# Kernel tuning notes

Measured on AMD Instinct MI355X. Metric: run time of the kernel, lower is better.

## Reference

```python
import jax, jax.numpy as jnp
import numpy as np

PAD_IDX = 0
B, T, S, H, V = 64, 32, 64, 1024, 32000


def setup_inputs() -> dict:
    key = jax.random.key(0)
    ks = jax.random.split(key, 12)
    s = 0.02
    emb_tbl = jax.random.normal(ks[0], (V, H), jnp.float32) * s
    emb_tbl = emb_tbl.at[PAD_IDX].set(0.0)  # padding_idx row is zero
    return {
        "input": jax.random.randint(ks[1], (B, T), 0, V),
        "memory": jax.random.normal(ks[2], (1, B, H), jnp.float32),
        "encoder_output": jax.random.normal(ks[3], (B, S, H), jnp.float32),
        "xs_len": jax.random.randint(ks[4], (B,), 1, S + 1),
        "embedding": emb_tbl,
        "w_ih": jax.random.normal(ks[5], (3 * H, 2 * H), jnp.float32) * s,
        "w_hh": jax.random.normal(ks[6], (3 * H, H), jnp.float32) * s,
        "b_ih": jnp.zeros((3 * H,), jnp.float32),
        "b_hh": jnp.zeros((3 * H,), jnp.float32),
        "l1": jax.random.normal(ks[7], (H, H), jnp.float32) * s,
        "l2": jax.random.normal(ks[8], (H, 2 * H), jnp.float32) * s,
        "w_out": jax.random.normal(ks[9], (V, H), jnp.float32) * s,
        "b_out": jnp.zeros((V,), jnp.float32),
    }


def _gru_cell(x, h, w_ih, w_hh, b_ih, b_hh):
    # torch.nn.GRUCell math
    gi = x @ w_ih.T + b_ih          # [B, 3H]
    gh = h @ w_hh.T + b_hh          # [B, 3H]
    ir, iz, inn = jnp.split(gi, 3, axis=1)
    hr, hz, hn = jnp.split(gh, 3, axis=1)
    r = jax.nn.sigmoid(ir + hr)
    z = jax.nn.sigmoid(iz + hz)
    n = jnp.tanh(inn + r * hn)
    return (1.0 - z) * n + z * h


def _attention(hidden, enc, seq_mask, l1, l2):
    # hidden: [B,H], enc: [B,S,H], seq_mask: [B,S] float {0,1}
    q = hidden @ l1.T                              # [B,H]
    score = jnp.einsum("bsh,bh->bs", enc, q)       # [B,S]
    masked = seq_mask * score
    # faithful to `masked_att[masked_att == 0] = -1e10`
    masked = jnp.where(masked == 0.0, -1e10, masked)
    attn = jax.nn.softmax(masked, axis=1)          # softmax over source positions
    ctx = jnp.einsum("bs,bsh->bh", attn, enc)      # [B,H]
    out = jnp.tanh(jnp.concatenate([ctx, hidden], axis=1) @ l2.T)
    return out, attn


def reference(input, memory, encoder_output, xs_len, embedding,
              w_ih, w_hh, b_ih, b_hh, l1, l2, w_out, b_out):
    emb = embedding[input]                         # [B,T,H]
    emb_t = jnp.swapaxes(emb, 0, 1)                # [T,B,H]
    h0 = memory[0]                                 # [B,H]
    ctx0 = jnp.zeros_like(h0)
    s_len = encoder_output.shape[1]
    seq_mask = (jnp.arange(s_len)[None, :] < xs_len[:, None]).astype(emb.dtype)  # [B,S]

    def step(carry, e_t):
        h_prev, ctx = carry
        x = jnp.concatenate([e_t, ctx], axis=1)    # [B,2H]
        h = _gru_cell(x, h_prev, w_ih, w_hh, b_ih, b_hh)
        ctx_new, attn = _attention(h, encoder_output, seq_mask, l1, l2)
        scores = jax.nn.log_softmax(ctx_new @ w_out.T + b_out, axis=1)  # [B,V]
        return (h, ctx_new), (scores, attn)

    (h_fin, ctx_fin), (all_scores, all_attn) = jax.lax.scan(step, (h0, ctx0), emb_t)
    decoder_output = jnp.swapaxes(all_scores, 0, 1)        # [B,T,V]
    decoder_hidden = h_fin[None, :, :]                     # [1,B,H]
    attention_weights = jnp.swapaxes(all_attn, 0, 1)       # [B,T,S]
    return decoder_output, decoder_hidden, attention_weights, ctx_fin
```

## Files before the change

kernel.cpp:

```cpp
#include <hip/hip_runtime.h>


#define B_ 64
#define T_ 32
#define S_ 64
#define H_ 1024
#define V_ 32000
#define NB_ 256
#define LDS_BYTES 152064

#define HID_OFF 65536000L
#define ATT_OFF 65601536L
#define CTF_OFF 65732608L

typedef __attribute__((ext_vector_type(8))) short bf16x8;
typedef __attribute__((ext_vector_type(4))) float f32x4;
typedef __attribute__((ext_vector_type(4))) unsigned int u32x4;
typedef unsigned short u16;
typedef unsigned long long u64;

__device__ __forceinline__ u16 f2bf(float v) {
  unsigned int u = __float_as_uint(v);
  unsigned int r = (u + 0x7fffu + ((u >> 16) & 1u)) >> 16;
  return (u16)r;
}
__device__ __forceinline__ float bf2f(u16 h) {
  return __uint_as_float(((unsigned int)h) << 16);
}
__device__ __forceinline__ void split2(float v, u16* hi, u16* lo) {
  u16 h = f2bf(v);
  *hi = h;
  *lo = f2bf(v - bf2f(h));
}

__device__ __forceinline__ u64 aload_u64(const void* p) {
  return __hip_atomic_load((const u64*)p, __ATOMIC_RELAXED, __HIP_MEMORY_SCOPE_AGENT);
}
__device__ __forceinline__ unsigned aload_u32(const void* p) {
  return __hip_atomic_load((const unsigned*)p, __ATOMIC_RELAXED, __HIP_MEMORY_SCOPE_AGENT);
}
__device__ __forceinline__ void astore_u64(void* p, u64 v) {
  __hip_atomic_store((u64*)p, v, __ATOMIC_RELAXED, __HIP_MEMORY_SCOPE_AGENT);
}
__device__ __forceinline__ void astore_f32(float* p, float v) {
  __hip_atomic_store((unsigned*)p, __float_as_uint(v), __ATOMIC_RELAXED,
                     __HIP_MEMORY_SCOPE_AGENT);
}


__global__ void k_split(const float* __restrict__ src, u16* __restrict__ hi,
                        u16* __restrict__ lo, int n) {
  int i = blockIdx.x * blockDim.x + threadIdx.x;
  int stride = gridDim.x * blockDim.x;
  for (; i < n; i += stride) split2(src[i], &hi[i], &lo[i]);
}

__global__ void k_tobf(const float* __restrict__ src, u16* __restrict__ dst, int n) {
  int i = blockIdx.x * blockDim.x + threadIdx.x;
  int stride = gridDim.x * blockDim.x;
  for (; i < n; i += stride) dst[i] = f2bf(src[i]);
}

__global__ void k_l1t(const float* __restrict__ l1, u16* __restrict__ hi,
                      u16* __restrict__ lo) {
  __shared__ float tile[64][65];
  int it = blockIdx.x & 15, kt = blockIdx.x >> 4;
  for (int q = 0; q < 16; ++q) {
    int idx = q * 256 + threadIdx.x;
    int r = idx >> 6, c = idx & 63;
    tile[r][c] = l1[(long)(it * 64 + r) * H_ + kt * 64 + c];
  }
  __syncthreads();
  for (int q = 0; q < 16; ++q) {
    int idx = q * 256 + threadIdx.x;
    int r = idx >> 6, c = idx & 63;
    long o = (long)(kt * 64 + r) * H_ + it * 64 + c;
    split2(tile[c][r], &hi[o], &lo[o]);
  }
}

__global__ void k_embx(const int* __restrict__ inp, const float* __restrict__ emb,
                       u16* __restrict__ hi, u16* __restrict__ lo) {
  int bt = blockIdx.x;
  int b = bt >> 5, t = bt & 31;
  int id = inp[b * T_ + t];
  const float* src = emb + (long)id * H_;
  long base = (long)(t * B_ + b) * H_;
  for (int k = threadIdx.x; k < H_; k += 256) split2(src[k], &hi[base + k], &lo[base + k]);
}

__global__ void k_h0(const float* __restrict__ mem, u16* __restrict__ hh,
                     u16* __restrict__ hl) {
  int i = blockIdx.x * 256 + threadIdx.x;
  float v = mem[i];
  split2(v, &hh[i], &hl[i]);
}

__global__ void k_guard(float* out, float v) {
  if (blockIdx.x == 0 && threadIdx.x == 0) out[0] = v;
}

template <int SPLIT, int OMODE>
__launch_bounds__(256)
__global__ void k_gemm128(const u16* __restrict__ Ah, const u16* __restrict__ Al,
                          const u16* __restrict__ Bh, const u16* __restrict__ Bl,
                          float* __restrict__ C, const float* __restrict__ bias,
                          int Mtiles, int Ntiles, int K, int Arow, int Brow, int Crow) {
  (void)Ntiles;
  int bx = blockIdx.x;
  int mt = bx % Mtiles, nt = bx / Mtiles;
  int m0 = mt * 128, n0 = nt * 128;

  __shared__ __attribute__((aligned(16))) u16 lds[(SPLIT ? 4 : 2) * 4096];
  char* L = (char*)lds;
  const int tid = threadIdx.x;
  const int lane = tid & 63, wid = tid >> 6;
  const int wm = wid & 1, wn = wid >> 1;
  const int l15 = lane & 15, kq = lane >> 4;

  f32x4 acc[4][4];
  const f32x4 z4 = {0.f, 0.f, 0.f, 0.f};
#pragma unroll
  for (int i = 0; i < 4; ++i)
#pragma unroll
    for (int j = 0; j < 4; ++j) acc[i][j] = z4;

  const int ksteps = K >> 5;
  for (int kt = 0; kt < ksteps; ++kt) {
    __syncthreads();
#pragma unroll
    for (int h2 = 0; h2 < 2; ++h2) {
      int r = (tid >> 2) + (h2 << 6);
      int slot = tid & 3;
      int so = ((slot ^ (r & 3)) << 4);
      long ga = (long)(m0 + r) * Arow + (kt << 5) + (slot << 3);
      long gb = (long)(n0 + r) * Brow + (kt << 5) + (slot << 3);
      *(u32x4*)(L + r * 64 + so) = *(const u32x4*)(Ah + ga);
      *(u32x4*)(L + 8192 + r * 64 + so) = *(const u32x4*)(Bh + gb);
      if (SPLIT) {
        *(u32x4*)(L + 16384 + r * 64 + so) = *(const u32x4*)(Al + ga);
        *(u32x4*)(L + 24576 + r * 64 + so) = *(const u32x4*)(Bl + gb);
      }
    }
    __syncthreads();
    bf16x8 aH[4], bH[4], aL[4], bL[4];
#pragma unroll
    for (int mi = 0; mi < 4; ++mi) {
      int r = (wm << 6) + (mi << 4) + l15;
      int off = r * 64 + ((kq ^ (r & 3)) << 4);
      aH[mi] = *(const bf16x8*)(L + off);
      if (SPLIT) aL[mi] = *(const bf16x8*)(L + 16384 + off);
    }
#pragma unroll
    for (int ni = 0; ni < 4; ++ni) {
      int c = (wn << 6) + (ni << 4) + l15;
      int off = c * 64 + ((kq ^ (c & 3)) << 4);
      bH[ni] = *(const bf16x8*)(L + 8192 + off);
      if (SPLIT) bL[ni] = *(const bf16x8*)(L + 24576 + off);
    }
#pragma unroll
    for (int mi = 0; mi < 4; ++mi)
#pragma unroll
      for (int ni = 0; ni < 4; ++ni) {
        acc[mi][ni] = __builtin_amdgcn_mfma_f32_16x16x32_bf16(aH[mi], bH[ni], acc[mi][ni], 0, 0, 0);
        if (SPLIT) {
          acc[mi][ni] = __builtin_amdgcn_mfma_f32_16x16x32_bf16(aL[mi], bH[ni], acc[mi][ni], 0, 0, 0);
          acc[mi][ni] = __builtin_amdgcn_mfma_f32_16x16x32_bf16(aH[mi], bL[ni], acc[mi][ni], 0, 0, 0);
        }
      }
  }
#pragma unroll
  for (int mi = 0; mi < 4; ++mi)
#pragma unroll
    for (int ni = 0; ni < 4; ++ni)
#pragma unroll
      for (int e = 0; e < 4; ++e) {
        int r = (wm << 6) + (mi << 4) + (kq << 2) + e;
        int c = (wn << 6) + (ni << 4) + l15;
        int gm = m0 + r, gn = n0 + c;
        float v = acc[mi][ni][e];
        if (OMODE == 0) {
          C[(long)gm * Crow + gn] = v;
        } else {
          v += bias[gn];
          C[((long)(gm & 63) * T_ + (gm >> 6)) * V_ + gn] = v;
        }
      }
}

__device__ __forceinline__ void gridbar(unsigned* flags, unsigned seq) {
  __syncthreads();
  if (threadIdx.x == 0) {
    unsigned g = blockIdx.x & 7u;
    unsigned old = __hip_atomic_fetch_add(flags + g * 64, 1u, __ATOMIC_RELEASE,
                                          __HIP_MEMORY_SCOPE_AGENT);
    if (old == seq * 32u - 1u) {
      unsigned o2 = __hip_atomic_fetch_add(flags + 1024, 1u, __ATOMIC_RELEASE,
                                           __HIP_MEMORY_SCOPE_AGENT);
      if (o2 == seq * 8u - 1u)
        __hip_atomic_store(flags + 1040, seq, __ATOMIC_RELAXED,
                           __HIP_MEMORY_SCOPE_AGENT);
    }
    while (__hip_atomic_load(flags + 1040, __ATOMIC_RELAXED,
                             __HIP_MEMORY_SCOPE_AGENT) < seq)
      __builtin_amdgcn_s_sleep(2);
  }
  __syncthreads();
}

__launch_bounds__(256)
__global__ void k_rec(const float* __restrict__ embi,
                      u16* __restrict__ dctx_h, u16* __restrict__ dctx_l,
                      u16* __restrict__ hh_r, u16* __restrict__ hl_r,
                      const float* __restrict__ memory,
                      const u16* __restrict__ wih_h, const u16* __restrict__ wih_l,
                      const u16* __restrict__ whh_h, const u16* __restrict__ whh_l,
                      const u16* __restrict__ l2_h, const u16* __restrict__ l2_l,
                      float* __restrict__ gip, float* __restrict__ ghp,
                      float* __restrict__ psc, float* __restrict__ ctxp,
                      const float* __restrict__ encT, const float* __restrict__ encL,
                      const int* __restrict__ xs_len,
                      const float* __restrict__ bih, const float* __restrict__ bhh,
                      float* __restrict__ dout, unsigned* flags) {
  extern __shared__ __attribute__((aligned(16))) char L[];
  char* W_HI = L;
  char* W_LO = L + 65536;
  char* A_HI = L + 131072;
  char* A_LO = L + 139264;
  float* hq = (float*)(L + 147456);
  float* at_s = (float*)(L + 148480);
  const int bx = blockIdx.x;
  const int tid = threadIdx.x;
  const int lane = tid & 63, wid = tid >> 6;
  const int wm = wid & 1, wn = wid >> 1;
  const int l15 = lane & 15, kq = lane >> 4;
  const f32x4 z4 = {0.f, 0.f, 0.f, 0.f};
  unsigned seq = 1;

  const int isGI = (bx < 96);
  const int isGH = (bx >= 96 && bx < 192);
  const int isL2 = (bx >= 192 && bx < 224);
  const int sb = bx >> 2;
  const int sq = bx & 3;
  int nt = 0, kc = 0, n0 = 0;
  const u16 *Wg_h = nullptr, *Wg_l = nullptr;
  int wrs = 0;
  if (isGI) {
    nt = bx % 48; kc = bx / 48;
    Wg_h = wih_h + 1024 + (long)nt * 64 * 2048 + kc * 512;
    Wg_l = wih_l + 1024 + (long)nt * 64 * 2048 + kc * 512;
    wrs = 2048;
  } else if (isGH) {
    int j2 = bx - 96;
    nt = j2 % 48; kc = j2 / 48;
    Wg_h = whh_h + (long)nt * 64 * 1024 + kc * 512;
    Wg_l = whh_l + (long)nt * 64 * 1024 + kc * 512;
    wrs = 1024;
  } else if (isL2) {
    n0 = (bx - 192) << 5;
    Wg_h = l2_h + 1024 + (long)n0 * 2048;
    Wg_l = l2_l + 1024 + (long)n0 * 2048;
    wrs = 2048;
  }

  if (isGI || isGH) {
    for (int e = tid; e < 4096; e += 256) {
      int st = e >> 8, r = (e >> 2) & 63, slot = e & 3;
      long g = (long)r * wrs + st * 32 + slot * 8;
      int o = st * 4096 + r * 64 + ((slot ^ (r & 3)) << 4);
      *(u32x4*)(W_HI + o) = *(const u32x4*)(Wg_h + g);
      *(u32x4*)(W_LO + o) = *(const u32x4*)(Wg_l + g);
    }
  } else if (isL2) {
    for (int e = tid; e < 4096; e += 256) {
      int st = e >> 7, r = (e >> 2) & 31, slot = e & 3;
      long g = (long)r * wrs + st * 32 + slot * 8;
      int o = st * 2048 + r * 64 + ((slot ^ (r & 3)) << 4);
      *(u32x4*)(W_HI + o) = *(const u32x4*)(Wg_h + g);
      *(u32x4*)(W_LO + o) = *(const u32x4*)(Wg_l + g);
    }
  }
  __syncthreads();

  float hpv = memory[sb * 1024 + sq * 256 + tid];

  const int pr = tid >> 2, ps = tid & 3;
  const int ao = pr * 64 + ((ps ^ (pr & 3)) << 4);

  for (int t = 0; t < T_; ++t) {
    if (isGI || isGH) {
      const u16* Ah;
      const u16* Al;
      float* outp;
      if (isGI) {
        Ah = dctx_h + (long)t * 65536 + kc * 512;
        Al = dctx_l + (long)t * 65536 + kc * 512;
        outp = gip + (long)kc * 196608 + nt * 64;
      } else {
        Ah = hh_r + (long)t * 65536 + kc * 512;
        Al = hl_r + (long)t * 65536 + kc * 512;
        outp = ghp + (long)kc * 196608 + nt * 64;
      }
      const long g0 = (long)pr * 1024 + ps * 8;
      u32x4 ph0 = *(const u32x4*)(Ah + g0);
      u32x4 ph1 = *(const u32x4*)(Ah + g0 + 32);
      u32x4 pl0 = *(const u32x4*)(Al + g0);
      u32x4 pl1 = *(const u32x4*)(Al + g0 + 32);

      f32x4 acc[2][2];
#pragma unroll
      for (int i = 0; i < 2; ++i)
#pragma unroll
        for (int j = 0; j < 2; ++j) acc[i][j] = z4;

      for (int kt = 0; kt < 8; ++kt) {
        __syncthreads();
        *(u32x4*)(A_HI + ao) = ph0;
        *(u32x4*)(A_HI + 4096 + ao) = ph1;
        *(u32x4*)(A_LO + ao) = pl0;
        *(u32x4*)(A_LO + 4096 + ao) = pl1;
        __syncthreads();
        if (kt < 7) {
          long g = g0 + (kt + 1) * 64;
          ph0 = *(const u32x4*)(Ah + g);
          ph1 = *(const u32x4*)(Ah + g + 32);
          pl0 = *(const u32x4*)(Al + g);
          pl1 = *(const u32x4*)(Al + g + 32);
        }
#pragma unroll
        for (int sub = 0; sub < 2; ++sub) {
          const int stw = (kt * 2 + sub) * 4096;
          const int sta = sub * 4096;
          bf16x8 aH[2], aL[2], bH[2], bL[2];
#pragma unroll
          for (int mi = 0; mi < 2; ++mi) {
            int rr = (wm << 5) + (mi << 4) + l15;
            int off = rr * 64 + ((kq ^ (rr & 3)) << 4);
            aH[mi] = *(const bf16x8*)(A_HI + sta + off);
            aL[mi] = *(const bf16x8*)(A_LO + sta + off);
          }
#pragma unroll
          for (int ni = 0; ni < 2; ++ni) {
            int c = (wn << 5) + (ni << 4) + l15;
            int off = c * 64 + ((kq ^ (c & 3)) << 4);
            bH[ni] = *(const bf16x8*)(W_HI + stw + off);
            bL[ni] = *(const bf16x8*)(W_LO + stw + off);
          }
#pragma unroll
          for (int mi = 0; mi < 2; ++mi)
#pragma unroll
            for (int ni = 0; ni < 2; ++ni) {
              acc[mi][ni] = __builtin_amdgcn_mfma_f32_16x16x32_bf16(aH[mi], bH[ni], acc[mi][ni], 0, 0, 0);
              acc[mi][ni] = __builtin_amdgcn_mfma_f32_16x16x32_bf16(aL[mi], bH[ni], acc[mi][ni], 0, 0, 0);
              acc[mi][ni] = __builtin_amdgcn_mfma_f32_16x16x32_bf16(aH[mi], bL[ni], acc[mi][ni], 0, 0, 0);
            }
        }
      }
#pragma unroll
      for (int mi = 0; mi < 2; ++mi)
#pragma unroll
        for (int ni = 0; ni < 2; ++ni)
#pragma unroll
          for (int e = 0; e < 4; ++e) {
            int r = (wm << 5) + (mi << 4) + (kq << 2) + e;
            int c = (wn << 5) + (ni << 4) + l15;
            astore_f32(outp + (long)r * 3072 + c, acc[mi][ni][e]);
          }
    }
    gridbar(flags, seq); seq++;

    {
      const int b = sb, q = sq;
      const int j = (q << 8) + tid;
      const float* eb = embi + ((long)t * 64 + b) * 3072;
      float g0r = __uint_as_float(aload_u32(gip + b * 3072 + j));
      float g1r = __uint_as_float(aload_u32(gip + 196608 + b * 3072 + j));
      float g0z = __uint_as_float(aload_u32(gip + b * 3072 + 1024 + j));
      float g1z = __uint_as_float(aload_u32(gip + 196608 + b * 3072 + 1024 + j));
      float g0n = __uint_as_float(aload_u32(gip + b * 3072 + 2048 + j));
      float g1n = __uint_as_float(aload_u32(gip + 196608 + b * 3072 + 2048 + j));
      float h0r = __uint_as_float(aload_u32(ghp + b * 3072 + j));
      float h1r = __uint_as_float(aload_u32(ghp + 196608 + b * 3072 + j));
      float h0z = __uint_as_float(aload_u32(ghp + b * 3072 + 1024 + j));
      float h1z = __uint_as_float(aload_u32(ghp + 196608 + b * 3072 + 1024 + j));
      float h0n = __uint_as_float(aload_u32(ghp + b * 3072 + 2048 + j));
      float h1n = __uint_as_float(aload_u32(ghp + 196608 + b * 3072 + 2048 + j));
      float ir = eb[j] + g0r + g1r + bih[j];
      float iz = eb[1024 + j] + g0z + g1z + bih[1024 + j];
      float in2 = eb[2048 + j] + g0n + g1n + bih[2048 + j];
      float hr = h0r + h1r + bhh[j];
      float hz = h0z + h1z + bhh[1024 + j];
      float hn = h0n + h1n + bhh[2048 + j];
      float r = 1.f / (1.f + expf(-(ir + hr)));
      float z = 1.f / (1.f + expf(-(iz + hz)));
      float n = tanhf(in2 + r * hn);
      float h = (1.f - z) * n + z * hpv;
      hpv = h;
      hq[tid] = h;
      if (t == T_ - 1) dout[HID_OFF + (long)b * 1024 + j] = h;
      __syncthreads();
      if (tid < 64) {
        u64 ph = 0, pl = 0;
#pragma unroll
        for (int ii = 0; ii < 4; ++ii) {
          u16 hi, lo;
          split2(hq[tid * 4 + ii], &hi, &lo);
          ph |= (u64)hi << (16 * ii);
          pl |= (u64)lo << (16 * ii);
        }
        long o = (long)(t + 1) * 65536 + (long)b * 1024 + (q << 8) + tid * 4;
        astore_u64(hh_r + o, ph);
        astore_u64(hl_r + o, pl);
      }
      {
        int s = tid >> 2, part = tid & 3;
        const float4* ep = (const float4*)(encT + (((long)b * 64 + s) << 10) + (q << 8) + (part << 6));
        const float4* hp = (const float4*)(hq + (part << 6));
        float dot = 0.f;
#pragma unroll
        for (int kk = 0; kk < 16; ++kk) {
          float4 e = ep[kk], a = hp[kk];
          dot += e.x * a.x + e.y * a.y + e.z * a.z + e.w * a.w;
        }
        dot += __shfl_xor(dot, 1);
        dot += __shfl_xor(dot, 2);
        if (part == 0) astore_f32(psc + (((b << 2) + q) << 6) + s, dot);
      }
    }
    gridbar(flags, seq); seq++;

    {
      const int b = sb, q = sq;
      if (tid < 64) {
        int s = tid;
        float v = 0.f;
#pragma unroll
        for (int qq = 0; qq < 4; ++qq)
          v += __uint_as_float(aload_u32(psc + (((b << 2) + qq) << 6) + s));
        int len = xs_len[b];
        if (s >= len || v == 0.0f) v = -1e10f;
        float m = v;
#pragma unroll
        for (int off = 32; off; off >>= 1) m = fmaxf(m, __shfl_xor(m, off));
        float p = expf(v - m);
        float sum = p;
#pragma unroll
        for (int off = 32; off; off >>= 1) sum += __shfl_xor(sum, off);
        float a = p / sum;
        at_s[s] = a;
        if (q == 0) dout[ATT_OFF + ((long)b * T_ + t) * S_ + s] = a;
      }
      __syncthreads();
      {
        const float* lp = encL + (((long)b * 64 + (q << 4)) << 10) + tid * 4;
        float c0 = 0.f, c1 = 0.f, c2 = 0.f, c3 = 0.f;
#pragma unroll
        for (int s2 = 0; s2 < 16; ++s2) {
          float a = at_s[(q << 4) + s2];
          float4 e = *(const float4*)(lp + (s2 << 10));
          c0 += a * e.x; c1 += a * e.y; c2 += a * e.z; c3 += a * e.w;
        }
        u64 w0 = ((u64)__float_as_uint(c1) << 32) | __float_as_uint(c0);
        u64 w1 = ((u64)__float_as_uint(c3) << 32) | __float_as_uint(c2);
        long o = (((long)(b << 2) + q) << 10) + tid * 4;
        astore_u64(ctxp + o, w0);
        astore_u64(ctxp + o + 2, w1);
      }
    }
    gridbar(flags, seq); seq++;

    if (isL2) {
      const u16* Ah = hh_r + (long)(t + 1) * 65536;
      const u16* Al = hl_r + (long)(t + 1) * 65536;
      const long g0 = (long)pr * 1024 + ps * 8;
      u32x4 ph0 = *(const u32x4*)(Ah + g0);
      u32x4 ph1 = *(const u32x4*)(Ah + g0 + 32);
      u32x4 pl0 = *(const u32x4*)(Al + g0);
      u32x4 pl1 = *(const u32x4*)(Al + g0 + 32);

      f32x4 acc[2];
      acc[0] = z4; acc[1] = z4;
      for (int kt = 0; kt < 16; ++kt) {
        __syncthreads();
        *(u32x4*)(A_HI + ao) = ph0;
        *(u32x4*)(A_HI + 4096 + ao) = ph1;
        *(u32x4*)(A_LO + ao) = pl0;
        *(u32x4*)(A_LO + 4096 + ao) = pl1;
        __syncthreads();
        if (kt < 15) {
          long g = g0 + (kt + 1) * 64;
          ph0 = *(const u32x4*)(Ah + g);
          ph1 = *(const u32x4*)(Ah + g + 32);
          pl0 = *(const u32x4*)(Al + g);
          pl1 = *(const u32x4*)(Al + g + 32);
        }
#pragma unroll
        for (int sub = 0; sub < 2; ++sub) {
          const int stw = (kt * 2 + sub) * 2048;
          const int sta = sub * 4096;
          bf16x8 aH[2], aL[2], bH, bL;
#pragma unroll
          for (int mi = 0; mi < 2; ++mi) {
            int rr = (wm << 5) + (mi << 4) + l15;
            int off = rr * 64 + ((kq ^ (rr & 3)) << 4);
            aH[mi] = *(const bf16x8*)(A_HI + sta + off);
            aL[mi] = *(const bf16x8*)(A_LO + sta + off);
          }
          {
            int c = (wn << 4) + l15;
            int off = c * 64 + ((kq ^ (c & 3)) << 4);
            bH = *(const bf16x8*)(W_HI + stw + off);
            bL = *(const bf16x8*)(W_LO + stw + off);
          }
#pragma unroll
          for (int mi = 0; mi < 2; ++mi) {
            acc[mi] = __builtin_amdgcn_mfma_f32_16x16x32_bf16(aH[mi], bH, acc[mi], 0, 0, 0);
            acc[mi] = __builtin_amdgcn_mfma_f32_16x16x32_bf16(aL[mi], bH, acc[mi], 0, 0, 0);
            acc[mi] = __builtin_amdgcn_mfma_f32_16x16x32_bf16(aH[mi], bL, acc[mi], 0, 0, 0);
          }
        }
      }
      __syncthreads();
      float* cf = (float*)(L + 131072);
#pragma unroll
      for (int mi = 0; mi < 2; ++mi)
#pragma unroll
        for (int e = 0; e < 4; ++e) {
          int rr = (wm << 5) + (mi << 4) + (kq << 2) + e;
          int cc = (wn << 4) + l15;
          float a = 0.f;
#pragma unroll
          for (int qq = 0; qq < 4; ++qq)
            a += __uint_as_float(aload_u32(ctxp + (((long)(rr << 2) + qq) << 10) + n0 + cc));
          float v = tanhf(acc[mi][e] + a);
          if (t == T_ - 1) dout[CTF_OFF + (long)rr * 1024 + n0 + cc] = v;
          cf[rr * 32 + cc] = v;
        }
      __syncthreads();
#pragma unroll
      for (int qq2 = 0; qq2 < 2; ++qq2) {
        int g = tid + qq2 * 256;
        int b = g >> 3, colg = g & 7;
        u64 ph = 0, pl = 0;
#pragma unroll
        for (int ii = 0; ii < 4; ++ii) {
          float v = cf[b * 32 + colg * 4 + ii];
          u16 hi, lo;
          split2(v, &hi, &lo);
          ph |= (u64)hi << (16 * ii);
          pl |= (u64)lo << (16 * ii);
        }
        long o = (long)(t + 1) * 65536 + (long)b * 1024 + n0 + colg * 4;
        astore_u64(dctx_h + o, ph);
        astore_u64(dctx_l + o, pl);
      }
    }
    if (t < T_ - 1) { gridbar(flags, seq); }
    seq++;
  }
}

__device__ __forceinline__ void lse_comb(float& m, float& s, float mo, float so) {
  float M = fmaxf(m, mo);
  s = s * __expf(m - M) + so * __expf(mo - M);
  m = M;
}

__launch_bounds__(256)
__global__ void k_lsm(float* __restrict__ dout) {
  long base = (long)blockIdx.x * V_;
  int tid = threadIdx.x;
  float m = -3.0e38f, s = 0.f;
  for (int v = tid; v < V_; v += 256) {
    float x = dout[base + v];
    if (x > m) {
      s = s * __expf(m - x) + 1.f;
      m = x;
    } else {
      s += __expf(x - m);
    }
  }
#pragma unroll
  for (int off = 32; off; off >>= 1) {
    float mo = __shfl_xor(m, off), so = __shfl_xor(s, off);
    lse_comb(m, s, mo, so);
  }
  __shared__ float ms[4], ss[4];
  if ((tid & 63) == 0) { ms[tid >> 6] = m; ss[tid >> 6] = s; }
  __syncthreads();
  float M = ms[0], S = ss[0];
  for (int w2 = 1; w2 < 4; ++w2) lse_comb(M, S, ms[w2], ss[w2]);
  float logden = M + logf(S);
  for (int v = tid; v < V_; v += 256) dout[base + v] -= logden;
}

extern "C" void kernel_launch(void* const* d_in, const int* in_sizes, int n_in,
                              void* d_out, int out_size, void* d_ws, size_t ws_size,
                              hipStream_t stream) {
  (void)in_sizes; (void)n_in; (void)out_size;
  const int* input = (const int*)d_in[0];
  const float* memory = (const float*)d_in[1];
  const float* enc = (const float*)d_in[2];
  const int* xs_len = (const int*)d_in[3];
  const float* emb = (const float*)d_in[4];
  const float* wih = (const float*)d_in[5];
  const float* whh = (const float*)d_in[6];
  const float* bih = (const float*)d_in[7];
  const float* bhh = (const float*)d_in[8];
  const float* l1 = (const float*)d_in[9];
  const float* l2 = (const float*)d_in[10];
  const float* wout = (const float*)d_in[11];
  const float* bout = (const float*)d_in[12];
  float* out = (float*)d_out;
  char* w = (char*)d_ws;

  size_t off = 0;
  auto alloc = [&](size_t bytes) {
    size_t o = off;
    off = (off + bytes + 255) & ~(size_t)255;
    return o;
  };
  const size_t N_WIH = 3072UL * 2048, N_WHH = 3072UL * 1024, N_L2 = 1024UL * 2048;
  const size_t N_L1 = 1024UL * 1024, N_ENC = 4096UL * 1024, N_WOUT = 32000UL * 1024;
  const size_t N_EMBX = 2048UL * 1024, N_ENCT = 4096UL * 1024;
  const size_t N_EMBI = 2048UL * 3072, N_ROT = 33UL * 65536;

  size_t o_wih_h = alloc(2 * N_WIH), o_wih_l = alloc(2 * N_WIH);
  size_t o_whh_h = alloc(2 * N_WHH), o_whh_l = alloc(2 * N_WHH);
  size_t o_l2_h = alloc(2 * N_L2), o_l2_l = alloc(2 * N_L2);
  size_t o_l1t_h = alloc(2 * N_L1), o_l1t_l = alloc(2 * N_L1);
  size_t o_ctx_h = alloc(2 * N_ROT), o_ctx_l = alloc(2 * N_ROT);
  size_t o_hh = alloc(2 * N_ROT), o_hl = alloc(2 * N_ROT);
  size_t o_gip = alloc(4 * 2 * 196608), o_ghp = alloc(4 * 2 * 196608);
  size_t o_psc = alloc(4 * 16384);
  size_t o_ctxp = alloc(4 * 262144);
  size_t o_bar = alloc(16384);
  size_t o_arena = alloc(2 * N_ENC * 2 + 2 * N_EMBX * 2 + 4 * N_EMBI + 4 * N_ENCT * 2);

  if (off > ws_size) {
    k_guard<<<1, 1, 0, stream>>>(out, 1.0e8f + (float)(ws_size >> 20));
    return;
  }

  u16* wih_h = (u16*)(w + o_wih_h);   u16* wih_l = (u16*)(w + o_wih_l);
  u16* whh_h = (u16*)(w + o_whh_h);   u16* whh_l = (u16*)(w + o_whh_l);
  u16* l2_h = (u16*)(w + o_l2_h);     u16* l2_l = (u16*)(w + o_l2_l);
  u16* l1t_h = (u16*)(w + o_l1t_h);   u16* l1t_l = (u16*)(w + o_l1t_l);
  u16* ctx_h = (u16*)(w + o_ctx_h);   u16* ctx_l = (u16*)(w + o_ctx_l);
  u16* hh_r = (u16*)(w + o_hh);       u16* hl_r = (u16*)(w + o_hl);
  float* gip = (float*)(w + o_gip);
  float* ghp = (float*)(w + o_ghp);
  float* psc = (float*)(w + o_psc);
  float* ctxp = (float*)(w + o_ctxp);
  unsigned* flags = (unsigned*)(w + o_bar);

  char* ar = w + o_arena;
  u16* enc_h = (u16*)ar;
  u16* enc_l = (u16*)(ar + 2 * N_ENC);
  u16* embx_h = (u16*)(ar + 4 * N_ENC);
  u16* embx_l = (u16*)(ar + 4 * N_ENC + 2 * N_EMBX);
  float* embi = (float*)(ar + 4 * N_ENC + 4 * N_EMBX);
  float* encT = (float*)(ar + 4 * N_ENC + 4 * N_EMBX + 4 * N_EMBI);
  float* encL = (float*)(ar + 4 * N_ENC + 4 * N_EMBX + 4 * N_EMBI + 4 * N_ENCT);
  u16* wout_b = (u16*)ar;

  hipFuncSetAttribute((const void*)k_rec, hipFuncAttributeMaxDynamicSharedMemorySize,
                      LDS_BYTES);

  k_split<<<2048, 256, 0, stream>>>(wih, wih_h, wih_l, (int)N_WIH);
  k_split<<<2048, 256, 0, stream>>>(whh, whh_h, whh_l, (int)N_WHH);
  k_split<<<2048, 256, 0, stream>>>(l2, l2_h, l2_l, (int)N_L2);
  k_split<<<2048, 256, 0, stream>>>(enc, enc_h, enc_l, (int)N_ENC);
  k_l1t<<<256, 256, 0, stream>>>(l1, l1t_h, l1t_l);
  k_embx<<<2048, 256, 0, stream>>>(input, emb, embx_h, embx_l);
  k_h0<<<256, 256, 0, stream>>>(memory, hh_r, hl_r);
  hipMemsetAsync(ctx_h, 0, 131072, stream);
  hipMemsetAsync(ctx_l, 0, 131072, stream);
  hipMemsetAsync(flags, 0, 16384, stream);

  k_gemm128<1, 0><<<256, 256, 0, stream>>>(enc_h, enc_l, l1t_h, l1t_l, encT, nullptr,
                                           32, 8, 1024, 1024, 1024, 1024);
  k_gemm128<1, 0><<<256, 256, 0, stream>>>(enc_h, enc_l, l2_h, l2_l, encL, nullptr,
                                           32, 8, 1024, 1024, 2048, 1024);
  k_gemm128<1, 0><<<384, 256, 0, stream>>>(embx_h, embx_l, wih_h, wih_l, embi, nullptr,
                                           16, 24, 1024, 1024, 2048, 3072);

  k_rec<<<NB_, 256, LDS_BYTES, stream>>>(embi, ctx_h, ctx_l, hh_r, hl_r, memory,
                                         wih_h, wih_l, whh_h, whh_l, l2_h, l2_l,
                                         gip, ghp, psc, ctxp, encT, encL,
                                         xs_len, bih, bhh, out, flags);

  k_tobf<<<4096, 256, 0, stream>>>(wout, wout_b, (int)N_WOUT);

  k_gemm128<0, 1><<<4000, 256, 0, stream>>>(ctx_h + 65536, nullptr, wout_b, nullptr,
                                            out, bout, 16, 250, 1024, 1024, 1024, 0);
  k_lsm<<<2048, 256, 0, stream>>>(out);
}
```

Measured before the change: 2.041 ms.

## Overlap W_hh GEMM with L2 phase and split grid barrier into arrive/wait

Moves the next step's h@W_hh GEMM so it runs in the same phase as the L2 projection, which takes it off the critical path of the following GI phase. The grid barrier is split into arrive and wait halves, and dummy prefetch loads of the embedding and next-step operands are issued in the gap between them. The GEMM inner loop is factored into a template that double-buffers two K-tiles of register prefetch. Epilogue stores are packed into 64-bit writes via a lane shuffle. Correctness depends on the hidden state for step t+1 already being written before the third barrier.

After: 2.114 ms. +3.6%, slower.

```diff
diff --git a/kernel.cpp b/kernel.cpp
--- a/kernel.cpp
+++ b/kernel.cpp
@@ -188,7 +188,7 @@
       }
 }
 
-__device__ __forceinline__ void gridbar(unsigned* flags, unsigned seq) {
+__device__ __forceinline__ void gb_arrive(unsigned* flags, unsigned seq) {
   __syncthreads();
   if (threadIdx.x == 0) {
     unsigned g = blockIdx.x & 7u;
@@ -201,11 +201,134 @@
         __hip_atomic_store(flags + 1040, seq, __ATOMIC_RELAXED,
                            __HIP_MEMORY_SCOPE_AGENT);
     }
+  }
+}
+__device__ __forceinline__ void gb_wait(unsigned* flags, unsigned seq) {
+  if (threadIdx.x == 0) {
     while (__hip_atomic_load(flags + 1040, __ATOMIC_RELAXED,
                              __HIP_MEMORY_SCOPE_AGENT) < seq)
       __builtin_amdgcn_s_sleep(2);
   }
   __syncthreads();
+}
+__device__ __forceinline__ void gridbar(unsigned* flags, unsigned seq) {
+  gb_arrive(flags, seq);
+  gb_wait(flags, seq);
+}
+
+template <int NI, int NKT>
+__device__ __forceinline__ void gemm_slab(const u16* __restrict__ Ah,
+                                          const u16* __restrict__ Al,
+                                          char* W_HI, char* W_LO, char* A_HI,
+                                          char* A_LO, int wm, int wn, int l15,
+                                          int kq, int pr, int ps, int ao,
+                                          f32x4 (&acc)[2][NI]) {
+  const int wsub = (NI == 2) ? 4096 : 2048;
+  const long g0 = (long)pr * 1024 + ps * 8;
+  u32x4 pa0, pa1, pa2, pa3, pb0, pb1, pb2, pb3;
+  {
+    pa0 = *(const u32x4*)(Ah + g0);      pa1 = *(const u32x4*)(Ah + g0 + 32);
+    pa2 = *(const u32x4*)(Al + g0);      pa3 = *(const u32x4*)(Al + g0 + 32);
+    pb0 = *(const u32x4*)(Ah + g0 + 64); pb1 = *(const u32x4*)(Ah + g0 + 96);
+    pb2 = *(const u32x4*)(Al + g0 + 64); pb3 = *(const u32x4*)(Al + g0 + 96);
+  }
+#pragma unroll
+  for (int kt = 0; kt < NKT; kt += 2) {
+    __syncthreads();
+    *(u32x4*)(A_HI + ao) = pa0; *(u32x4*)(A_HI + 4096 + ao) = pa1;
+    *(u32x4*)(A_LO + ao) = pa2; *(u32x4*)(A_LO + 4096 + ao) = pa3;
+    __syncthreads();
+    if (kt + 2 < NKT) {
+      long g = g0 + (long)(kt + 2) * 64;
+      pa0 = *(const u32x4*)(Ah + g);      pa1 = *(const u32x4*)(Ah + g + 32);
+      pa2 = *(const u32x4*)(Al + g);      pa3 = *(const u32x4*)(Al + g + 32);
+    }
+#pragma unroll
+    for (int sub = 0; sub < 2; ++sub) {
+      const int stw = (kt * 2 + sub) * wsub;
+      const int sta = sub * 4096;
+      bf16x8 aH[2], aL[2], bH[NI], bL[NI];
+#pragma unroll
+      for (int mi = 0; mi < 2; ++mi) {
+        int rr = (wm << 5) + (mi << 4) + l15;
+        int off = rr * 64 + ((kq ^ (rr & 3)) << 4);
+        aH[mi] = *(const bf16x8*)(A_HI + sta + off);
+        aL[mi] = *(const bf16x8*)(A_LO + sta + off);
+      }
+#pragma unroll
+      for (int ni = 0; ni < NI; ++ni) {
+        int c = (wn << (NI == 2 ? 5 : 4)) + (ni << 4) + l15;
+        int off = c * 64 + ((kq ^ (c & 3)) << 4);
+        bH[ni] = *(const bf16x8*)(W_HI + stw + off);
+        bL[ni] = *(const bf16x8*)(W_LO + stw + off);
+      }
+#pragma unroll
+      for (int mi = 0; mi < 2; ++mi)
+#pragma unroll
+        for (int ni = 0; ni < NI; ++ni) {
+          acc[mi][ni] = __builtin_amdgcn_mfma_f32_16x16x32_bf16(aH[mi], bH[ni], acc[mi][ni], 0, 0, 0);
+          acc[mi][ni] = __builtin_amdgcn_mfma_f32_16x16x32_bf16(aL[mi], bH[ni], acc[mi][ni], 0, 0, 0);
+          acc[mi][ni] = __builtin_amdgcn_mfma_f32_16x16x32_bf16(aH[mi], bL[ni], acc[mi][ni], 0, 0, 0);
+        }
+    }
+    __syncthreads();
+    *(u32x4*)(A_HI + ao) = pb0; *(u32x4*)(A_HI + 4096 + ao) = pb1;
+    *(u32x4*)(A_LO + ao) = pb2; *(u32x4*)(A_LO + 4096 + ao) = pb3;
+    __syncthreads();
+    if (kt + 3 < NKT) {
+      long g = g0 + (long)(kt + 3) * 64;
+      pb0 = *(const u32x4*)(Ah + g);      pb1 = *(const u32x4*)(Ah + g + 32);
+      pb2 = *(const u32x4*)(Al + g);      pb3 = *(const u32x4*)(Al + g + 32);
+    }
+#pragma unroll
+    for (int sub = 0; sub < 2; ++sub) {
+      const int stw = ((kt + 1) * 2 + sub) * wsub;
+      const int sta = sub * 4096;
+      bf16x8 aH[2], aL[2], bH[NI], bL[NI];
+#pragma unroll
+      for (int mi = 0; mi < 2; ++mi) {
+        int rr = (wm << 5) + (mi << 4) + l15;
+        int off = rr * 64 + ((kq ^ (rr & 3)) << 4);
+        aH[mi] = *(const bf16x8*)(A_HI + sta + off);
+        aL[mi] = *(const bf16x8*)(A_LO + sta + off);
+      }
+#pragma unroll
+      for (int ni = 0; ni < NI; ++ni) {
+        int c = (wn << (NI == 2 ? 5 : 4)) + (ni << 4) + l15;
+        int off = c * 64 + ((kq ^ (c & 3)) << 4);
+        bH[ni] = *(const bf16x8*)(W_HI + stw + off);
+        bL[ni] = *(const bf16x8*)(W_LO + stw + off);
+      }
+#pragma unroll
+      for (int mi = 0; mi < 2; ++mi)
+#pragma unroll
+        for (int ni = 0; ni < NI; ++ni) {
+          acc[mi][ni] = __builtin_amdgcn_mfma_f32_16x16x32_bf16(aH[mi], bH[ni], acc[mi][ni], 0, 0, 0);
+          acc[mi][ni] = __builtin_amdgcn_mfma_f32_16x16x32_bf16(aL[mi], bH[ni], acc[mi][ni], 0, 0, 0);
+          acc[mi][ni] = __builtin_amdgcn_mfma_f32_16x16x32_bf16(aH[mi], bL[ni], acc[mi][ni], 0, 0, 0);
+        }
+    }
+  }
+}
+
+__device__ __forceinline__ void epi_pack(float* __restrict__ outp,
+                                         f32x4 (&acc)[2][2], int wm, int wn,
+                                         int l15, int kq) {
+#pragma unroll
+  for (int mi = 0; mi < 2; ++mi)
+#pragma unroll
+    for (int ni = 0; ni < 2; ++ni)
+#pragma unroll
+      for (int e = 0; e < 4; ++e) {
+        int r = (wm << 5) + (mi << 4) + (kq << 2) + e;
+        int c = (wn << 5) + (ni << 4) + l15;
+        float v = acc[mi][ni][e];
+        float o = __shfl_xor(v, 1);
+        if (!(l15 & 1)) {
+          u64 pk = ((u64)__float_as_uint(o) << 32) | __float_as_uint(v);
+          astore_u64(outp + (long)r * 3072 + c, pk);
+        }
+      }
 }
 
 __launch_bounds__(256)
@@ -286,88 +409,37 @@
 
   const int pr = tid >> 2, ps = tid & 3;
   const int ao = pr * 64 + ((ps ^ (pr & 3)) << 4);
+  const long g0w = (long)pr * 1024 + ps * 8;
 
   for (int t = 0; t < T_; ++t) {
-    if (isGI || isGH) {
-      const u16* Ah;
-      const u16* Al;
-      float* outp;
-      if (isGI) {
-        Ah = dctx_h + (long)t * 65536 + kc * 512;
-        Al = dctx_l + (long)t * 65536 + kc * 512;
-        outp = gip + (long)kc * 196608 + nt * 64;
-      } else {
-        Ah = hh_r + (long)t * 65536 + kc * 512;
-        Al = hl_r + (long)t * 65536 + kc * 512;
-        outp = ghp + (long)kc * 196608 + nt * 64;
-      }
-      const long g0 = (long)pr * 1024 + ps * 8;
-      u32x4 ph0 = *(const u32x4*)(Ah + g0);
-      u32x4 ph1 = *(const u32x4*)(Ah + g0 + 32);
-      u32x4 pl0 = *(const u32x4*)(Al + g0);
-      u32x4 pl1 = *(const u32x4*)(Al + g0 + 32);
-
+    if (isGI) {
       f32x4 acc[2][2];
 #pragma unroll
       for (int i = 0; i < 2; ++i)
 #pragma unroll
         for (int j = 0; j < 2; ++j) acc[i][j] = z4;
-
-      for (int kt = 0; kt < 8; ++kt) {
-        __syncthreads();
-        *(u32x4*)(A_HI + ao) = ph0;
-        *(u32x4*)(A_HI + 4096 + ao) = ph1;
-        *(u32x4*)(A_LO + ao) = pl0;
-        *(u32x4*)(A_LO + 4096 + ao) = pl1;
-        __syncthreads();
-        if (kt < 7) {
-          long g = g0 + (kt + 1) * 64;
-          ph0 = *(const u32x4*)(Ah + g);
-          ph1 = *(const u32x4*)(Ah + g + 32);
-          pl0 = *(const u32x4*)(Al + g);
-          pl1 = *(const u32x4*)(Al + g + 32);
-        }
-#pragma unroll
-        for (int sub = 0; sub < 2; ++sub) {
-          const int stw = (kt * 2 + sub) * 4096;
-          const int sta = sub * 4096;
-          bf16x8 aH[2], aL[2], bH[2], bL[2];
-#pragma unroll
-          for (int mi = 0; mi < 2; ++mi) {
-            int rr = (wm << 5) + (mi << 4) + l15;
-            int off = rr * 64 + ((kq ^ (rr & 3)) << 4);
-            aH[mi] = *(const bf16x8*)(A_HI + sta + off);
-            aL[mi] = *(const bf16x8*)(A_LO + sta + off);
-          }
-#pragma unroll
-          for (int ni = 0; ni < 2; ++ni) {
-            int c = (wn << 5) + (ni << 4) + l15;
-            int off = c * 64 + ((kq ^ (c & 3)) << 4);
-            bH[ni] = *(const bf16x8*)(W_HI + stw + off);
-            bL[ni] = *(const bf16x8*)(W_LO + stw + off);
-          }
-#pragma unroll
-          for (int mi = 0; mi < 2; ++mi)
-#pragma unroll
-            for (int ni = 0; ni < 2; ++ni) {
-              acc[mi][ni] = __builtin_amdgcn_mfma_f32_16x16x32_bf16(aH[mi], bH[ni], acc[mi][ni], 0, 0, 0);
-              acc[mi][ni] = __builtin_amdgcn_mfma_f32_16x16x32_bf16(aL[mi], bH[ni], acc[mi][ni], 0, 0, 0);
-              acc[mi][ni] = __builtin_amdgcn_mfma_f32_16x16x32_bf16(aH[mi], bL[ni], acc[mi][ni], 0, 0, 0);
-            }
-        }
-      }
-#pragma unroll
-      for (int mi = 0; mi < 2; ++mi)
-#pragma unroll
-        for (int ni = 0; ni < 2; ++ni)
-#pragma unroll
-          for (int e = 0; e < 4; ++e) {
-            int r = (wm << 5) + (mi << 4) + (kq << 2) + e;
-            int c = (wn << 5) + (ni << 4) + l15;
-            astore_f32(outp + (long)r * 3072 + c, acc[mi][ni][e]);
-          }
-    }
-    gridbar(flags, seq); seq++;
+      gemm_slab<2, 8>(dctx_h + (long)t * 65536 + kc * 512,
+                      dctx_l + (long)t * 65536 + kc * 512,
+                      W_HI, W_LO, A_HI, A_LO, wm, wn, l15, kq, pr, ps, ao, acc);
+      epi_pack(gip + (long)kc * 196608 + nt * 64, acc, wm, wn, l15, kq);
+    } else if (isGH && t == 0) {
+      f32x4 acc[2][2];
+#pragma unroll
+      for (int i = 0; i < 2; ++i)
+#pragma unroll
+        for (int j = 0; j < 2; ++j) acc[i][j] = z4;
+      gemm_slab<2, 8>(hh_r + kc * 512, hl_r + kc * 512,
+                      W_HI, W_LO, A_HI, A_LO, wm, wn, l15, kq, pr, ps, ao, acc);
+      epi_pack(ghp + (long)kc * 196608 + nt * 64, acc, wm, wn, l15, kq);
+    }
+    gb_arrive(flags, seq);
+    {
+      const float* eb = embi + ((long)t * 64 + sb) * 3072;
+      int j = (sq << 8) + tid;
+      float w0 = eb[j], w1 = eb[1024 + j], w2 = eb[2048 + j];
+      asm volatile("" :: "v"(w0), "v"(w1), "v"(w2));
+    }
+    gb_wait(flags, seq); seq++;
 
     {
       const int b = sb, q = sq;
@@ -467,59 +539,23 @@
         astore_u64(ctxp + o + 2, w1);
       }
     }
-    gridbar(flags, seq); seq++;
+    gb_arrive(flags, seq);
+    if (isL2 || (isGH && t < T_ - 1)) {
+      const u16* wa_h = hh_r + (long)(t + 1) * 65536 + (isGH ? kc * 512 : 0);
+      const u16* wa_l = hl_r + (long)(t + 1) * 65536 + (isGH ? kc * 512 : 0);
+      unsigned t0 = *(const u16*)(wa_h + g0w);
+      unsigned t1 = *(const u16*)(wa_l + g0w);
+      unsigned t2 = *(const u16*)(wa_h + g0w + 64);
+      unsigned t3 = *(const u16*)(wa_l + g0w + 64);
+      asm volatile("" :: "v"(t0), "v"(t1), "v"(t2), "v"(t3));
+    }
+    gb_wait(flags, seq); seq++;
 
     if (isL2) {
-      const u16* Ah = hh_r + (long)(t + 1) * 65536;
-      const u16* Al = hl_r + (long)(t + 1) * 65536;
-      const long g0 = (long)pr * 1024 + ps * 8;
-      u32x4 ph0 = *(const u32x4*)(Ah + g0);
-      u32x4 ph1 = *(const u32x4*)(Ah + g0 + 32);
-      u32x4 pl0 = *(const u32x4*)(Al + g0);
-      u32x4 pl1 = *(const u32x4*)(Al + g0 + 32);
-
-      f32x4 acc[2];
-      acc[0] = z4; acc[1] = z4;
-      for (int kt = 0; kt < 16; ++kt) {
-        __syncthreads();
-        *(u32x4*)(A_HI + ao) = ph0;
-        *(u32x4*)(A_HI + 4096 + ao) = ph1;
-        *(u32x4*)(A_LO + ao) = pl0;
-        *(u32x4*)(A_LO + 4096 + ao) = pl1;
-        __syncthreads();
-        if (kt < 15) {
-          long g = g0 + (kt + 1) * 64;
-          ph0 = *(const u32x4*)(Ah + g);
-          ph1 = *(const u32x4*)(Ah + g + 32);
-          pl0 = *(const u32x4*)(Al + g);
-          pl1 = *(const u32x4*)(Al + g + 32);
-        }
-#pragma unroll
-        for (int sub = 0; sub < 2; ++sub) {
-          const int stw = (kt * 2 + sub) * 2048;
-          const int sta = sub * 4096;
-          bf16x8 aH[2], aL[2], bH, bL;
-#pragma unroll
-          for (int mi = 0; mi < 2; ++mi) {
-            int rr = (wm << 5) + (mi << 4) + l15;
-            int off = rr * 64 + ((kq ^ (rr & 3)) << 4);
-            aH[mi] = *(const bf16x8*)(A_HI + sta + off);
-            aL[mi] = *(const bf16x8*)(A_LO + sta + off);
-          }
-          {
-            int c = (wn << 4) + l15;
-            int off = c * 64 + ((kq ^ (c & 3)) << 4);
-            bH = *(const bf16x8*)(W_HI + stw + off);
-            bL = *(const bf16x8*)(W_LO + stw + off);
-          }
-#pragma unroll
-          for (int mi = 0; mi < 2; ++mi) {
-            acc[mi] = __builtin_amdgcn_mfma_f32_16x16x32_bf16(aH[mi], bH, acc[mi], 0, 0, 0);
-            acc[mi] = __builtin_amdgcn_mfma_f32_16x16x32_bf16(aL[mi], bH, acc[mi], 0, 0, 0);
-            acc[mi] = __builtin_amdgcn_mfma_f32_16x16x32_bf16(aH[mi], bL, acc[mi], 0, 0, 0);
-          }
-        }
-      }
+      f32x4 acc[2][1];
+      acc[0][0] = z4; acc[1][0] = z4;
+      gemm_slab<1, 16>(hh_r + (long)(t + 1) * 65536, hl_r + (long)(t + 1) * 65536,
+                       W_HI, W_LO, A_HI, A_LO, wm, wn, l15, kq, pr, ps, ao, acc);
       __syncthreads();
       float* cf = (float*)(L + 131072);
 #pragma unroll
@@ -532,7 +568,7 @@
 #pragma unroll
           for (int qq = 0; qq < 4; ++qq)
             a += __uint_as_float(aload_u32(ctxp + (((long)(rr << 2) + qq) << 10) + n0 + cc));
-          float v = tanhf(acc[mi][e] + a);
+          float v = tanhf(acc[mi][0][e] + a);
           if (t == T_ - 1) dout[CTF_OFF + (long)rr * 1024 + n0 + cc] = v;
           cf[rr * 32 + cc] = v;
         }
@@ -554,6 +590,16 @@
         astore_u64(dctx_h + o, ph);
         astore_u64(dctx_l + o, pl);
       }
+    } else if (isGH && t < T_ - 1) {
+      f32x4 acc[2][2];
+#pragma unroll
+      for (int i = 0; i < 2; ++i)
+#pragma unroll
+        for (int j = 0; j < 2; ++j) acc[i][j] = z4;
+      gemm_slab<2, 8>(hh_r + (long)(t + 1) * 65536 + kc * 512,
+                      hl_r + (long)(t + 1) * 65536 + kc * 512,
+                      W_HI, W_LO, A_HI, A_LO, wm, wn, l15, kq, pr, ps, ao, acc);
+      epi_pack(ghp + (long)kc * 196608 + nt * 64, acc, wm, wn, l15, kq);
     }
     if (t < T_ - 1) { gridbar(flags, seq); }
     seq++;
```
